# Optimization experiments

Hardware: AMD Instinct MI355X
Metric: run time of the kernel (lower is better)

Reference implementation:

```python
import jax, jax.numpy as jnp
import numpy as np

B, S, H = 4, 4096, 2048
G, EPG = 4, 16            # num_expert_groups, experts_per_group
E = G * EPG               # num_experts = 64
TOP_K = 2
TOP_GROUPS = min(2, G)


def setup_inputs() -> dict:
    key = jax.random.key(0)
    ks = jax.random.split(key, 6)
    sc = 0.02
    return {
        "x": jax.random.normal(ks[0], (B, S, H), dtype=jnp.float32),
        "Wg": jax.random.normal(ks[1], (H, G), dtype=jnp.float32) * sc,
        "bg": jnp.zeros((G,), jnp.float32),
        "We": jax.random.normal(ks[2], (G, H, EPG), dtype=jnp.float32) * sc,
        "be": jnp.zeros((G, EPG), jnp.float32),
        "Wc1": jax.random.normal(ks[3], (H, H // 4), dtype=jnp.float32) * sc,
        "bc1": jnp.zeros((H // 4,), jnp.float32),
        "Wc2": jax.random.normal(ks[4], (H // 4, 1), dtype=jnp.float32) * sc,
        "bc2": jnp.zeros((1,), jnp.float32),
        "priority": jnp.ones((E,), jnp.float32).at[::EPG].set(1.2),
    }


def reference(x, Wg, bg, We, be, Wc1, bc1, Wc2, bc2, priority):
    N = B * S
    xf = x.reshape(N, H)

    # confidence estimator: Linear -> GELU(exact) -> Linear -> Sigmoid, [N,1]
    conf = jax.nn.sigmoid(jax.nn.gelu(xf @ Wc1 + bc1, approximate=False) @ Wc2 + bc2)

    # group routing (eval mode: no jitter)
    group_probs = jax.nn.softmax(xf @ Wg + bg, axis=-1)          # [N,G]
    tg_probs, tg_idx = jax.lax.top_k(group_probs, TOP_GROUPS)    # [N,2]

    # expert logits for ALL groups at once (grouped GEMM), scaled by priority
    logits = jnp.einsum('nh,ghe->nge', xf, We) + be              # [N,G,EPG]
    logits = logits * priority.reshape(G, EPG)
    probs = jax.nn.softmax(logits, axis=-1)                      # [N,G,EPG]
    c = conf[:, :, None]                                         # [N,1,1]
    probs = probs * c + (1.0 - c) / EPG                          # confidence mixing

    k = min(TOP_K, EPG)
    rows = jnp.arange(N)
    expert_scores = jnp.zeros((N, E), x.dtype)
    # top-2 selected groups are distinct -> global expert indices disjoint -> set is safe
    for g in range(TOP_GROUPS):
        gid = tg_idx[:, g]                                       # [N]
        pg = jnp.take_along_axis(probs, gid[:, None, None], axis=1)[:, 0, :]  # [N,EPG]
        tp, ti = jax.lax.top_k(pg, k)                            # [N,k]
        glob = ti + gid[:, None] * EPG                           # global expert ids
        w = tp * tg_probs[:, g:g + 1]                            # weight by group prob
        expert_scores = expert_scores.at[rows[:, None], glob].set(w)

    expert_scores = expert_scores / (expert_scores.sum(-1, keepdims=True) + 1e-9)

    ts, ti2 = jax.lax.top_k(expert_scores, TOP_K)                # [N,TOP_K]
    dispatch = jnp.zeros_like(expert_scores).at[rows[:, None], ti2].set(ts)
    dispatch = dispatch.reshape(B, S, E)
    combine = dispatch  # torch clones; identical values
    aux_loss = jnp.asarray(0.0, x.dtype)  # eval mode
    return dispatch, combine, aux_loss
```

## Files before the change

kernel.cpp:

```cpp
#include <hip/hip_runtime.h>

#define NTOK 16384
#define HDIM 2048
#define HD4  512
#define NG   4
#define EPG  16
#define NE   64

__global__ __launch_bounds__(256) void gemm_conf_kernel(
    const float* __restrict__ x, const float* __restrict__ Wc1,
    const float* __restrict__ bc1, float* __restrict__ h)
{
    __shared__ float As[16][132];
    __shared__ float Bs[16][132];
    const int tid = threadIdx.x;
    const int bm = blockIdx.x;
    const int bn = blockIdx.y;
    const int tr = tid >> 4, tc = tid & 15;

    float acc[8][8];
#pragma unroll
    for (int i = 0; i < 8; ++i)
#pragma unroll
        for (int j = 0; j < 8; ++j) acc[i][j] = 0.0f;

    const float* xb = x + (size_t)bm * 128 * HDIM;
    const float* wb = Wc1 + bn * 128;

    for (int k0 = 0; k0 < HDIM; k0 += 16) {
#pragma unroll
        for (int i = 0; i < 2; ++i) {
            int f4i = tid + i * 256;
            int arow = f4i >> 2, ak4 = f4i & 3;
            float4 v = *(const float4*)(xb + (size_t)arow * HDIM + k0 + ak4 * 4);
            As[ak4 * 4 + 0][arow] = v.x;
            As[ak4 * 4 + 1][arow] = v.y;
            As[ak4 * 4 + 2][arow] = v.z;
            As[ak4 * 4 + 3][arow] = v.w;
        }
#pragma unroll
        for (int i = 0; i < 2; ++i) {
            int f4i = tid + i * 256;
            int brow = f4i >> 5, bc4 = f4i & 31;
            *(float4*)&Bs[brow][bc4 * 4] =
                *(const float4*)(wb + (size_t)(k0 + brow) * HD4 + bc4 * 4);
        }
        __syncthreads();
#pragma unroll
        for (int k = 0; k < 16; ++k) {
            float av[8], bv[8];
            *(float4*)&av[0] = *(const float4*)&As[k][tr * 8];
            *(float4*)&av[4] = *(const float4*)&As[k][tr * 8 + 4];
            *(float4*)&bv[0] = *(const float4*)&Bs[k][tc * 8];
            *(float4*)&bv[4] = *(const float4*)&Bs[k][tc * 8 + 4];
#pragma unroll
            for (int i = 0; i < 8; ++i)
#pragma unroll
                for (int j = 0; j < 8; ++j)
                    acc[i][j] = fmaf(av[i], bv[j], acc[i][j]);
        }
        __syncthreads();
    }

    const int col0 = bn * 128 + tc * 8;
    float bb[8];
#pragma unroll
    for (int j = 0; j < 8; ++j) bb[j] = bc1[col0 + j];
#pragma unroll
    for (int i = 0; i < 8; ++i) {
        const int row = bm * 128 + tr * 8 + i;
        float o[8];
#pragma unroll
        for (int j = 0; j < 8; ++j) {
            float v = acc[i][j] + bb[j];
            o[j] = 0.5f * v * (1.0f + erff(v * 0.70710678118654752440f));
        }
        float* dst = h + (size_t)row * HD4 + col0;
        *(float4*)(dst)     = *(float4*)&o[0];
        *(float4*)(dst + 4) = *(float4*)&o[4];
    }
}

__global__ __launch_bounds__(256) void conf_reduce_kernel(
    const float* __restrict__ h, const float* __restrict__ Wc2,
    const float* __restrict__ bc2, float* __restrict__ conf)
{
    const int wv = threadIdx.x >> 6, lane = threadIdx.x & 63;
    const int n = blockIdx.x * 4 + wv;
    const float* hr = h + (size_t)n * HD4;
    float s = 0.0f;
#pragma unroll
    for (int t = 0; t < 2; ++t) {
        const int j = t * 256 + lane * 4;
        float4 hv = *(const float4*)(hr + j);
        float4 w4 = *(const float4*)(Wc2 + j);
        s = fmaf(hv.x, w4.x, s);
        s = fmaf(hv.y, w4.y, s);
        s = fmaf(hv.z, w4.z, s);
        s = fmaf(hv.w, w4.w, s);
    }
#pragma unroll
    for (int m = 32; m; m >>= 1) s += __shfl_xor(s, m, 64);
    if (lane == 0) {
        float v = s + bc2[0];
        conf[n] = 1.0f / (1.0f + expf(-v));
    }
}

__global__ __launch_bounds__(256) void gemm_experts_kernel(
    const float* __restrict__ x, const float* __restrict__ We,
    float* __restrict__ El)
{
    __shared__ float As[16][68];
    __shared__ float Bs[16][68];
    const int tid = threadIdx.x;
    const int bm = blockIdx.x;
    const int tr = tid >> 4, tc = tid & 15;

    float acc[4][4];
#pragma unroll
    for (int i = 0; i < 4; ++i)
#pragma unroll
        for (int j = 0; j < 4; ++j) acc[i][j] = 0.0f;

    const float* xb = x + (size_t)bm * 64 * HDIM;
    const int arow = tid >> 2, ak4 = tid & 3;
    const int bkk = tid >> 4;
    const int bgrp = (tid >> 2) & 3;
    const int be4 = tid & 3;

    for (int k0 = 0; k0 < HDIM; k0 += 16) {
        float4 va = *(const float4*)(xb + (size_t)arow * HDIM + k0 + ak4 * 4);
        As[ak4 * 4 + 0][arow] = va.x;
        As[ak4 * 4 + 1][arow] = va.y;
        As[ak4 * 4 + 2][arow] = va.z;
        As[ak4 * 4 + 3][arow] = va.w;
        *(float4*)&Bs[bkk][bgrp * 16 + be4 * 4] =
            *(const float4*)(We + (size_t)bgrp * HDIM * EPG
                             + (size_t)(k0 + bkk) * EPG + be4 * 4);
        __syncthreads();

        float acc_t[4][4];
#pragma unroll
        for (int i = 0; i < 4; ++i)
#pragma unroll
            for (int j = 0; j < 4; ++j) acc_t[i][j] = 0.0f;
#pragma unroll
        for (int k = 0; k < 16; ++k) {
            float av[4], bv[4];
            *(float4*)av = *(const float4*)&As[k][tr * 4];
            *(float4*)bv = *(const float4*)&Bs[k][tc * 4];
#pragma unroll
            for (int i = 0; i < 4; ++i)
#pragma unroll
                for (int j = 0; j < 4; ++j)
                    acc_t[i][j] = fmaf(av[i], bv[j], acc_t[i][j]);
        }
#pragma unroll
        for (int i = 0; i < 4; ++i)
#pragma unroll
            for (int j = 0; j < 4; ++j) acc[i][j] += acc_t[i][j];
        __syncthreads();
    }
#pragma unroll
    for (int i = 0; i < 4; ++i) {
        float o[4] = {acc[i][0], acc[i][1], acc[i][2], acc[i][3]};
        *(float4*)(El + (size_t)(bm * 64 + tr * 4 + i) * NE + tc * 4) = *(float4*)o;
    }
}

__global__ __launch_bounds__(256) void gemv_gates_kernel(
    const float* __restrict__ x, const float* __restrict__ Wg,
    float* __restrict__ Gl)
{
    const int wv = threadIdx.x >> 6, lane = threadIdx.x & 63;
    const int n = blockIdx.x * 4 + wv;
    const float* xr = x + (size_t)n * HDIM;
    float a0 = 0, a1 = 0, a2 = 0, a3 = 0;
#pragma unroll
    for (int t = 0; t < 8; ++t) {
        const int k = t * 256 + lane * 4;
        float4 xv = *(const float4*)(xr + k);
        float4 w0 = *(const float4*)(Wg + (size_t)k * NG);
        float4 w1 = *(const float4*)(Wg + (size_t)k * NG + 4);
        float4 w2 = *(const float4*)(Wg + (size_t)k * NG + 8);
        float4 w3 = *(const float4*)(Wg + (size_t)k * NG + 12);
        a0 = fmaf(xv.x, w0.x, a0); a0 = fmaf(xv.y, w1.x, a0);
        a0 = fmaf(xv.z, w2.x, a0); a0 = fmaf(xv.w, w3.x, a0);
        a1 = fmaf(xv.x, w0.y, a1); a1 = fmaf(xv.y, w1.y, a1);
        a1 = fmaf(xv.z, w2.y, a1); a1 = fmaf(xv.w, w3.y, a1);
        a2 = fmaf(xv.x, w0.z, a2); a2 = fmaf(xv.y, w1.z, a2);
        a2 = fmaf(xv.z, w2.z, a2); a2 = fmaf(xv.w, w3.z, a2);
        a3 = fmaf(xv.x, w0.w, a3); a3 = fmaf(xv.y, w1.w, a3);
        a3 = fmaf(xv.z, w2.w, a3); a3 = fmaf(xv.w, w3.w, a3);
    }
#pragma unroll
    for (int m = 32; m; m >>= 1) {
        a0 += __shfl_xor(a0, m, 64);
        a1 += __shfl_xor(a1, m, 64);
        a2 += __shfl_xor(a2, m, 64);
        a3 += __shfl_xor(a3, m, 64);
    }
    if (lane == 0) {
        float4 r; r.x = a0; r.y = a1; r.z = a2; r.w = a3;
        *(float4*)(Gl + (size_t)n * NG) = r;
    }
}

__global__ __launch_bounds__(256) void finalize_kernel(
    const float* __restrict__ El, const float* __restrict__ Gl,
    const float* __restrict__ conf, const float* __restrict__ bgp,
    const float* __restrict__ bep, const float* __restrict__ prp,
    float* __restrict__ out)
{
    const int n = blockIdx.x * 256 + threadIdx.x;

    float gl0 = Gl[(size_t)n * NG + 0] + bgp[0];
    float gl1 = Gl[(size_t)n * NG + 1] + bgp[1];
    float gl2 = Gl[(size_t)n * NG + 2] + bgp[2];
    float gl3 = Gl[(size_t)n * NG + 3] + bgp[3];
    float gm = fmaxf(fmaxf(gl0, gl1), fmaxf(gl2, gl3));
    float e0 = expf(gl0 - gm), e1 = expf(gl1 - gm);
    float e2 = expf(gl2 - gm), e3 = expf(gl3 - gm);
    float gs = e0 + e1 + e2 + e3;
    float gp0 = e0 / gs, gp1 = e1 / gs, gp2 = e2 / gs, gp3 = e3 / gs;

    int g0 = 0; float t0 = gp0;
    if (gp1 > t0) { t0 = gp1; g0 = 1; }
    if (gp2 > t0) { t0 = gp2; g0 = 2; }
    if (gp3 > t0) { t0 = gp3; g0 = 3; }
    int g1 = -1; float t1 = -1.0f;
    if (g0 != 0)              { t1 = gp0; g1 = 0; }
    if (g0 != 1 && gp1 > t1)  { t1 = gp1; g1 = 1; }
    if (g0 != 2 && gp2 > t1)  { t1 = gp2; g1 = 2; }
    if (g0 != 3 && gp3 > t1)  { t1 = gp3; g1 = 3; }

    const float c = conf[n];
    const float uni = (1.0f - c) * (1.0f / 16.0f);

    int ci0, ci1, ci2, ci3;
    float cv0, cv1, cv2, cv3;

    auto proc = [&](int gid, float tp, int& ia, float& va, int& ib, float& vb) {
        const float* base = El + (size_t)n * NE + gid * EPG;
        const float* beb = bep + gid * EPG;
        const float* prb = prp + gid * EPG;
        float lv[16];
#pragma unroll
        for (int e = 0; e < 16; ++e) lv[e] = (base[e] + beb[e]) * prb[e];
        float m = lv[0];
#pragma unroll
        for (int e = 1; e < 16; ++e) m = fmaxf(m, lv[e]);
        float pe[16]; float s = 0.0f;
#pragma unroll
        for (int e = 0; e < 16; ++e) { pe[e] = expf(lv[e] - m); s += pe[e]; }
        const float cs = c / s;
        float bl[16];
#pragma unroll
        for (int e = 0; e < 16; ++e) bl[e] = fmaf(pe[e], cs, uni);
        int i0 = 0; float v0 = bl[0];
#pragma unroll
        for (int e = 1; e < 16; ++e) { if (bl[e] > v0) { v0 = bl[e]; i0 = e; } }
        int i1 = -1; float v1 = -1e30f;
#pragma unroll
        for (int e = 0; e < 16; ++e) {
            if (e != i0 && bl[e] > v1) { v1 = bl[e]; i1 = e; }
        }
        ia = gid * EPG + i0; va = v0 * tp;
        ib = gid * EPG + i1; vb = v1 * tp;
    };
    proc(g0, t0, ci0, cv0, ci1, cv1);
    proc(g1, t1, ci2, cv2, ci3, cv3);

    const float wsum = cv0 + cv1 + cv2 + cv3;
    const float winv = 1.0f / (wsum + 1e-9f);
    const float s0 = cv0 * winv, s1 = cv1 * winv;
    const float s2 = cv2 * winv, s3 = cv3 * winv;

    float bv = s0; int bi = ci0; int bslot = 0;
    if (s1 > bv || (s1 == bv && ci1 < bi)) { bv = s1; bi = ci1; bslot = 1; }
    if (s2 > bv || (s2 == bv && ci2 < bi)) { bv = s2; bi = ci2; bslot = 2; }
    if (s3 > bv || (s3 == bv && ci3 < bi)) { bv = s3; bi = ci3; bslot = 3; }
    float sv = -1.0f; int si = 1 << 30;
    if (bslot != 0 && (s0 > sv || (s0 == sv && ci0 < si))) { sv = s0; si = ci0; }
    if (bslot != 1 && (s1 > sv || (s1 == sv && ci1 < si))) { sv = s1; si = ci1; }
    if (bslot != 2 && (s2 > sv || (s2 == sv && ci2 < si))) { sv = s2; si = ci2; }
    if (bslot != 3 && (s3 > sv || (s3 == sv && ci3 < si))) { sv = s3; si = ci3; }

    float* d0 = out + (size_t)n * NE;
    float* d1 = out + (size_t)NTOK * NE + (size_t)n * NE;
#pragma unroll
    for (int q = 0; q < 16; ++q) {
        const int j = q * 4;
        float4 v;
        v.x = (j + 0 == bi) ? bv : ((j + 0 == si) ? sv : 0.0f);
        v.y = (j + 1 == bi) ? bv : ((j + 1 == si) ? sv : 0.0f);
        v.z = (j + 2 == bi) ? bv : ((j + 2 == si) ? sv : 0.0f);
        v.w = (j + 3 == bi) ? bv : ((j + 3 == si) ? sv : 0.0f);
        *(float4*)(d0 + j) = v;
        *(float4*)(d1 + j) = v;
    }
    if (n == 0) out[(size_t)2 * NTOK * NE] = 0.0f;
}

extern "C" void kernel_launch(void* const* d_in, const int* in_sizes, int n_in,
                              void* d_out, int out_size, void* d_ws, size_t ws_size,
                              hipStream_t stream)
{
    const float* x    = (const float*)d_in[0];
    const float* Wg   = (const float*)d_in[1];
    const float* bg   = (const float*)d_in[2];
    const float* We   = (const float*)d_in[3];
    const float* be   = (const float*)d_in[4];
    const float* Wc1  = (const float*)d_in[5];
    const float* bc1  = (const float*)d_in[6];
    const float* Wc2  = (const float*)d_in[7];
    const float* bc2  = (const float*)d_in[8];
    const float* prio = (const float*)d_in[9];
    float* out = (float*)d_out;

    float* h    = (float*)d_ws;
    float* conf = h + (size_t)NTOK * HD4;
    float* El   = conf + NTOK;
    float* Gl   = El + (size_t)NTOK * NE;

    gemm_conf_kernel<<<dim3(NTOK / 128, HD4 / 128), 256, 0, stream>>>(x, Wc1, bc1, h);
    conf_reduce_kernel<<<NTOK / 4, 256, 0, stream>>>(h, Wc2, bc2, conf);
    gemm_experts_kernel<<<NTOK / 64, 256, 0, stream>>>(x, We, El);
    gemv_gates_kernel<<<NTOK / 4, 256, 0, stream>>>(x, Wg, Gl);
    finalize_kernel<<<NTOK / 256, 256, 0, stream>>>(El, Gl, conf, bg, be, prio, out);
}
```

Before: 765.7 us.

## Retile confidence GEMM with register-streamed weights and split-K expert GEMM

The confidence GEMM now uses 64-row tiles, double-buffers the activation tile in shared memory with a register prefetch, and streams Wc1 straight from global memory into registers instead of staging it in shared memory. This drops one barrier per k-step and doubles the grid size. The expert-logit GEMM is split four ways along K to add parallelism, writing partial sums into the unused h buffer, and a new reduction kernel adds them. The cost is an extra launch and extra partial-sum traffic, and Wc1 global loads that may be less coalesced.

Measured after the change: 1.205 ms. 57.4% more time.

```diff
diff --git a/kernel.cpp b/kernel.cpp
--- a/kernel.cpp
+++ b/kernel.cpp
@@ -6,60 +6,58 @@
 #define NG   4
 #define EPG  16
 #define NE   64
+#define KSPLIT 4
 
 __global__ __launch_bounds__(256) void gemm_conf_kernel(
     const float* __restrict__ x, const float* __restrict__ Wc1,
     const float* __restrict__ bc1, float* __restrict__ h)
 {
-    __shared__ float As[16][132];
-    __shared__ float Bs[16][132];
+    __shared__ float As[2][16][68];
     const int tid = threadIdx.x;
     const int bm = blockIdx.x;
     const int bn = blockIdx.y;
-    const int tr = tid >> 4, tc = tid & 15;
-
-    float acc[8][8];
-#pragma unroll
-    for (int i = 0; i < 8; ++i)
+    const int tr = tid >> 4;
+    const int tc = tid & 15;
+
+    float acc[4][8];
+#pragma unroll
+    for (int i = 0; i < 4; ++i)
 #pragma unroll
         for (int j = 0; j < 8; ++j) acc[i][j] = 0.0f;
 
-    const float* xb = x + (size_t)bm * 128 * HDIM;
-    const float* wb = Wc1 + bn * 128;
+    const int arow = tid >> 2;
+    const int ak4  = tid & 3;
+    const float* xrow = x + (size_t)(bm * 64 + arow) * HDIM + ak4 * 4;
+
+    const float* wb = Wc1 + bn * 128 + tc * 8;
+
+    float4 va = *(const float4*)(xrow);
+    int cur = 0;
 
     for (int k0 = 0; k0 < HDIM; k0 += 16) {
-#pragma unroll
-        for (int i = 0; i < 2; ++i) {
-            int f4i = tid + i * 256;
-            int arow = f4i >> 2, ak4 = f4i & 3;
-            float4 v = *(const float4*)(xb + (size_t)arow * HDIM + k0 + ak4 * 4);
-            As[ak4 * 4 + 0][arow] = v.x;
-            As[ak4 * 4 + 1][arow] = v.y;
-            As[ak4 * 4 + 2][arow] = v.z;
-            As[ak4 * 4 + 3][arow] = v.w;
-        }
-#pragma unroll
-        for (int i = 0; i < 2; ++i) {
-            int f4i = tid + i * 256;
-            int brow = f4i >> 5, bc4 = f4i & 31;
-            *(float4*)&Bs[brow][bc4 * 4] =
-                *(const float4*)(wb + (size_t)(k0 + brow) * HD4 + bc4 * 4);
-        }
+        As[cur][ak4 * 4 + 0][arow] = va.x;
+        As[cur][ak4 * 4 + 1][arow] = va.y;
+        As[cur][ak4 * 4 + 2][arow] = va.z;
+        As[cur][ak4 * 4 + 3][arow] = va.w;
+        if (k0 + 16 < HDIM) va = *(const float4*)(xrow + k0 + 16);
         __syncthreads();
-#pragma unroll
-        for (int k = 0; k < 16; ++k) {
-            float av[8], bv[8];
-            *(float4*)&av[0] = *(const float4*)&As[k][tr * 8];
-            *(float4*)&av[4] = *(const float4*)&As[k][tr * 8 + 4];
-            *(float4*)&bv[0] = *(const float4*)&Bs[k][tc * 8];
-            *(float4*)&bv[4] = *(const float4*)&Bs[k][tc * 8 + 4];
-#pragma unroll
-            for (int i = 0; i < 8; ++i)
+
+        const float* wk = wb + (size_t)k0 * HD4;
+#pragma unroll
+        for (int kk = 0; kk < 16; ++kk) {
+            float4 b0 = *(const float4*)(wk);
+            float4 b1 = *(const float4*)(wk + 4);
+            wk += HD4;
+            float4 a4 = *(const float4*)&As[cur][kk][tr * 4];
+            float av[4] = {a4.x, a4.y, a4.z, a4.w};
+            float bv[8] = {b0.x, b0.y, b0.z, b0.w, b1.x, b1.y, b1.z, b1.w};
+#pragma unroll
+            for (int i = 0; i < 4; ++i)
 #pragma unroll
                 for (int j = 0; j < 8; ++j)
                     acc[i][j] = fmaf(av[i], bv[j], acc[i][j]);
         }
-        __syncthreads();
+        cur ^= 1;
     }
 
     const int col0 = bn * 128 + tc * 8;
@@ -67,8 +65,8 @@
 #pragma unroll
     for (int j = 0; j < 8; ++j) bb[j] = bc1[col0 + j];
 #pragma unroll
-    for (int i = 0; i < 8; ++i) {
-        const int row = bm * 128 + tr * 8 + i;
+    for (int i = 0; i < 4; ++i) {
+        const int row = bm * 64 + tr * 4 + i;
         float o[8];
 #pragma unroll
         for (int j = 0; j < 8; ++j) {
@@ -109,12 +107,13 @@
 
 __global__ __launch_bounds__(256) void gemm_experts_kernel(
     const float* __restrict__ x, const float* __restrict__ We,
-    float* __restrict__ El)
+    float* __restrict__ Elp)
 {
     __shared__ float As[16][68];
     __shared__ float Bs[16][68];
     const int tid = threadIdx.x;
     const int bm = blockIdx.x;
+    const int ks = blockIdx.y;
     const int tr = tid >> 4, tc = tid & 15;
 
     float acc[4][4];
@@ -129,7 +128,9 @@
     const int bgrp = (tid >> 2) & 3;
     const int be4 = tid & 3;
 
-    for (int k0 = 0; k0 < HDIM; k0 += 16) {
+    const int kbeg = ks * (HDIM / KSPLIT);
+    const int kend = kbeg + (HDIM / KSPLIT);
+    for (int k0 = kbeg; k0 < kend; k0 += 16) {
         float4 va = *(const float4*)(xb + (size_t)arow * HDIM + k0 + ak4 * 4);
         As[ak4 * 4 + 0][arow] = va.x;
         As[ak4 * 4 + 1][arow] = va.y;
@@ -165,8 +166,25 @@
 #pragma unroll
     for (int i = 0; i < 4; ++i) {
         float o[4] = {acc[i][0], acc[i][1], acc[i][2], acc[i][3]};
-        *(float4*)(El + (size_t)(bm * 64 + tr * 4 + i) * NE + tc * 4) = *(float4*)o;
-    }
+        *(float4*)(Elp + ((size_t)ks * NTOK + bm * 64 + tr * 4 + i) * NE + tc * 4)
+            = *(float4*)o;
+    }
+}
+
+__global__ __launch_bounds__(256) void reduce_el_kernel(
+    const float* __restrict__ Elp, float* __restrict__ El)
+{
+    const size_t i = ((size_t)blockIdx.x * 256 + threadIdx.x) * 4;
+    float4 a = *(const float4*)(Elp + i);
+    float4 b = *(const float4*)(Elp + (size_t)1 * NTOK * NE + i);
+    float4 c = *(const float4*)(Elp + (size_t)2 * NTOK * NE + i);
+    float4 d = *(const float4*)(Elp + (size_t)3 * NTOK * NE + i);
+    float4 r;
+    r.x = ((a.x + b.x) + c.x) + d.x;
+    r.y = ((a.y + b.y) + c.y) + d.y;
+    r.z = ((a.z + b.z) + c.z) + d.z;
+    r.w = ((a.w + b.w) + c.w) + d.w;
+    *(float4*)(El + i) = r;
 }
 
 __global__ __launch_bounds__(256) void gemv_gates_kernel(
@@ -323,10 +341,12 @@
     float* conf = h + (size_t)NTOK * HD4;
     float* El   = conf + NTOK;
     float* Gl   = El + (size_t)NTOK * NE;
-
-    gemm_conf_kernel<<<dim3(NTOK / 128, HD4 / 128), 256, 0, stream>>>(x, Wc1, bc1, h);
+    float* Elp  = h;
+
+    gemm_conf_kernel<<<dim3(NTOK / 64, HD4 / 128), 256, 0, stream>>>(x, Wc1, bc1, h);
     conf_reduce_kernel<<<NTOK / 4, 256, 0, stream>>>(h, Wc2, bc2, conf);
-    gemm_experts_kernel<<<NTOK / 64, 256, 0, stream>>>(x, We, El);
+    gemm_experts_kernel<<<dim3(NTOK / 64, KSPLIT), 256, 0, stream>>>(x, We, Elp);
+    reduce_el_kernel<<<(NTOK * NE / 4) / 256, 256, 0, stream>>>(Elp, El);
     gemv_gates_kernel<<<NTOK / 4, 256, 0, stream>>>(x, Wg, Gl);
     finalize_kernel<<<NTOK / 256, 256, 0, stream>>>(El, Gl, conf, bg, be, prio, out);
 }
```
